# Optimization experiments

Measured on AMD Instinct MI355X. Metric: run time of the kernel, lower is better.

## Reference

```python
import jax, jax.numpy as jnp
import numpy as np

N_NODES = 50000
N_EDGES = 800000
DIM = 128
BN_EPS = 1e-5
GATE_EPS = 1e-6


def setup_inputs() -> dict:
    key = jax.random.key(0)
    ks = jax.random.split(key, 14)
    scale = 1.0 / np.sqrt(DIM)
    inp = {
        "h": jax.random.normal(ks[0], (N_NODES, DIM), dtype=jnp.float32),
        "e": jax.random.normal(ks[1], (N_EDGES, DIM), dtype=jnp.float32),
        "src": jax.random.randint(ks[2], (N_EDGES,), 0, N_NODES),
        "dst": jax.random.randint(ks[3], (N_EDGES,), 0, N_NODES),
        # Linear A, B, D, E (n_mlp_layer=1 -> single Linear each)
        "Wa": jax.random.uniform(ks[4], (DIM, DIM), jnp.float32, -scale, scale),
        "ba": jax.random.uniform(ks[5], (DIM,), jnp.float32, -scale, scale),
        "Wb": jax.random.uniform(ks[6], (DIM, DIM), jnp.float32, -scale, scale),
        "bb": jax.random.uniform(ks[7], (DIM,), jnp.float32, -scale, scale),
        "Wd": jax.random.uniform(ks[8], (DIM, DIM), jnp.float32, -scale, scale),
        "bd": jax.random.uniform(ks[9], (DIM,), jnp.float32, -scale, scale),
        "We": jax.random.uniform(ks[10], (DIM, DIM), jnp.float32, -scale, scale),
        "be": jax.random.uniform(ks[11], (DIM,), jnp.float32, -scale, scale),
        # BatchNorm1d affine params (fresh init: gamma=1, beta=0)
        "gamma": jnp.ones((DIM,), jnp.float32),
        "beta": jnp.zeros((DIM,), jnp.float32),
    }
    return inp


def reference(h, e, src, dst, Wa, ba, Wb, bb, Wd, bd, We, be, gamma, beta):
    N = h.shape[0]
    # dense node projections
    Ah = h @ Wa + ba
    Bh = h @ Wb + bb
    Dh = h @ Wd + bd
    Eh = h @ We + be
    # edge gather + sigmoid gate: e_ij = Dh[src] + Eh[dst]
    sigma = jax.nn.sigmoid(Dh[src] + Eh[dst])          # [E, D]
    # scatter-sum by destination node (variable degree)
    num = jax.ops.segment_sum(sigma * Bh[src], dst, num_segments=N)
    den = jax.ops.segment_sum(sigma, dst, num_segments=N) + GATE_EPS
    h_new = Ah + num / den
    # BatchNorm1d (training mode: biased batch statistics) + relu
    mean = jnp.mean(h_new, axis=0)
    var = jnp.mean(jnp.square(h_new - mean), axis=0)
    h_new = (h_new - mean) * jax.lax.rsqrt(var + BN_EPS) * gamma + beta
    h_new = jax.nn.relu(h_new)
    # residual=False (default), dropout=0.0 -> identity
    return h_new, e
```

## Files before the change

### kernel.cpp

```cpp
#include <hip/hip_runtime.h>
#include <hip/hip_bf16.h>

#define DIM 128
#define GATE_EPS 1e-6f
#define BN_EPS 1e-5f

typedef unsigned int u32;
typedef unsigned short u16;

__device__ __forceinline__ float bflo(u32 u) { return __uint_as_float(u << 16); }
__device__ __forceinline__ float bfhi(u32 u) { return __uint_as_float(u & 0xffff0000u); }

__device__ __forceinline__ u16 f2bf(float f) {
    u32 u = __float_as_uint(f);
    u32 r = (u + 0x7fffu + ((u >> 16) & 1u)) >> 16;
    return (u16)r;
}

__device__ __forceinline__ float loadF(const void* p, size_t i, int bf) {
    if (bf) return __uint_as_float(((u32)((const u16*)p)[i]) << 16);
    return ((const float*)p)[i];
}

__global__ void detect_dtype(const void* __restrict__ h, int* __restrict__ flag) {
    if (threadIdx.x == 0 && blockIdx.x == 0) {
        const u16* us = (const u16*)h;
        int cnt = 0;
        for (int i = 0; i < 256; ++i) {
            int e8 = (us[2 * i] >> 7) & 0xFF;
            if (e8 >= 0x60 && e8 <= 0x8F) ++cnt;
        }
        *flag = (cnt >= 192) ? 1 : 0;
    }
}

__global__ __launch_bounds__(256) void proj_gemm(
    const void* __restrict__ h,
    const void* __restrict__ W0, const void* __restrict__ b0,
    const void* __restrict__ W1, const void* __restrict__ b1,
    const void* __restrict__ W2, const void* __restrict__ b2,
    const void* __restrict__ W3, const void* __restrict__ b3,
    float* __restrict__ oAh, u32* __restrict__ oDB, u32* __restrict__ oEhb,
    int N, const int* __restrict__ flagp)
{
    const void* W; const void* bias;
    switch (blockIdx.y) {
        case 0:  W = W0; bias = b0; break;
        case 1:  W = W1; bias = b1; break;
        case 2:  W = W2; bias = b2; break;
        default: W = W3; bias = b3; break;
    }
    const int bf = *flagp;

    __shared__ float Hs[64][DIM + 4];
    __shared__ float Ws[16][DIM];

    const int t  = threadIdx.x;
    const int m0 = blockIdx.x * 64;

    if (bf) {
        for (int f = t; f < 1024; f += 256) {
            int r = f >> 4, c8 = f & 15;
            int gr = m0 + r;
            uint4 v = make_uint4(0u, 0u, 0u, 0u);
            if (gr < N) v = ((const uint4*)h)[(size_t)gr * 16 + c8];
            float* p = &Hs[r][c8 * 8];
            p[0] = bflo(v.x); p[1] = bfhi(v.x);
            p[2] = bflo(v.y); p[3] = bfhi(v.y);
            p[4] = bflo(v.z); p[5] = bfhi(v.z);
            p[6] = bflo(v.w); p[7] = bfhi(v.w);
        }
    } else {
        for (int f = t; f < 2048; f += 256) {
            int r = f >> 5, c4 = f & 31;
            int gr = m0 + r;
            float4 v = make_float4(0.f, 0.f, 0.f, 0.f);
            if (gr < N) v = ((const float4*)h)[(size_t)gr * 32 + c4];
            float* p = &Hs[r][c4 * 4];
            p[0] = v.x; p[1] = v.y; p[2] = v.z; p[3] = v.w;
        }
    }

    const int cg = t & 31;
    const int rg = t >> 5;

    float acc[8][4];
    #pragma unroll
    for (int i = 0; i < 8; ++i)
        #pragma unroll
        for (int j = 0; j < 4; ++j) acc[i][j] = 0.f;

    for (int kc = 0; kc < DIM; kc += 16) {
        __syncthreads();
        if (bf) {
            int r = t >> 4, c8 = t & 15;
            uint4 v = ((const uint4*)W)[(size_t)(kc + r) * 16 + c8];
            float* p = &Ws[r][c8 * 8];
            p[0] = bflo(v.x); p[1] = bfhi(v.x);
            p[2] = bflo(v.y); p[3] = bfhi(v.y);
            p[4] = bflo(v.z); p[5] = bfhi(v.z);
            p[6] = bflo(v.w); p[7] = bfhi(v.w);
        } else {
            for (int f = t; f < 512; f += 256) {
                int r = f >> 5, c4 = f & 31;
                float4 v = ((const float4*)W)[(size_t)(kc + r) * 32 + c4];
                float* p = &Ws[r][c4 * 4];
                p[0] = v.x; p[1] = v.y; p[2] = v.z; p[3] = v.w;
            }
        }
        __syncthreads();
        #pragma unroll
        for (int kk = 0; kk < 16; ++kk) {
            float4 w = *((const float4*)&Ws[kk][cg * 4]);
            #pragma unroll
            for (int i = 0; i < 8; ++i) {
                float hv = Hs[rg * 8 + i][kc + kk];
                acc[i][0] += hv * w.x;
                acc[i][1] += hv * w.y;
                acc[i][2] += hv * w.z;
                acc[i][3] += hv * w.w;
            }
        }
    }

    float bv[4];
    #pragma unroll
    for (int j = 0; j < 4; ++j) bv[j] = loadF(bias, cg * 4 + j, bf);

    const int y = blockIdx.y;
    #pragma unroll
    for (int i = 0; i < 8; ++i) {
        int gr = m0 + rg * 8 + i;
        if (gr < N) {
            float v0 = acc[i][0] + bv[0];
            float v1 = acc[i][1] + bv[1];
            float v2 = acc[i][2] + bv[2];
            float v3 = acc[i][3] + bv[3];
            if (y == 0) {
                ((float4*)oAh)[(size_t)gr * 32 + cg] = make_float4(v0, v1, v2, v3);
            } else {
                uint2 p;
                p.x = (u32)f2bf(v0) | ((u32)f2bf(v1) << 16);
                p.y = (u32)f2bf(v2) | ((u32)f2bf(v3) << 16);
                size_t idx;
                if (y == 1)      idx = (size_t)gr * 64 + 32 + cg;
                else if (y == 2) idx = (size_t)gr * 64 + cg;
                else             idx = (size_t)gr * 32 + cg;
                u32* base = (y == 3) ? oEhb : oDB;
                ((uint2*)base)[idx] = p;
            }
        }
    }
}

__global__ __launch_bounds__(256) void k_hist(const int* __restrict__ dst,
                                              int* __restrict__ deg, int E)
{
    int e = blockIdx.x * 256 + threadIdx.x;
    if (e < E) atomicAdd(&deg[dst[e]], 1);
}

__global__ __launch_bounds__(256) void k_scan1(const int* __restrict__ deg,
                                               int* __restrict__ rowstart,
                                               int* __restrict__ part, int N)
{
    __shared__ int s[256];
    int t = threadIdx.x;
    int i = blockIdx.x * 256 + t;
    int d = (i < N) ? deg[i] : 0;
    s[t] = d;
    __syncthreads();
    for (int off = 1; off < 256; off <<= 1) {
        int v = (t >= off) ? s[t - off] : 0;
        __syncthreads();
        s[t] += v;
        __syncthreads();
    }
    if (i < N) rowstart[i] = s[t] - d;
    if (t == 255) part[blockIdx.x] = s[255];
}

__global__ void k_scan2(int* __restrict__ part, int nb)
{
    __shared__ int s[256];
    int t = threadIdx.x;
    int d = (t < nb) ? part[t] : 0;
    s[t] = d;
    __syncthreads();
    for (int off = 1; off < 256; off <<= 1) {
        int v = (t >= off) ? s[t - off] : 0;
        __syncthreads();
        s[t] += v;
        __syncthreads();
    }
    if (t < nb) part[t] = s[t] - d;
}

__global__ __launch_bounds__(256) void k_scan3(int* __restrict__ rowstart,
                                               int* __restrict__ cursor,
                                               const int* __restrict__ part,
                                               int N, int E)
{
    int i = blockIdx.x * 256 + threadIdx.x;
    if (i < N) {
        int v = rowstart[i] + part[blockIdx.x];
        rowstart[i] = v;
        cursor[i] = v;
    }
    if (i == 0) rowstart[N] = E;
}

__global__ __launch_bounds__(256) void k_scatter(const int* __restrict__ src,
                                                 const int* __restrict__ dst,
                                                 int* __restrict__ cursor,
                                                 int* __restrict__ esrc, int E)
{
    int e = blockIdx.x * 256 + threadIdx.x;
    if (e < E) {
        int pos = atomicAdd(&cursor[dst[e]], 1);
        esrc[pos] = src[e];
    }
}

__global__ __launch_bounds__(256) void k_aggregate(
    const float* __restrict__ Ah, const u32* __restrict__ DB,
    const u32* __restrict__ Ehb,
    const int* __restrict__ rowstart, const int* __restrict__ esrc,
    float* __restrict__ hnew, float* __restrict__ gsum, float* __restrict__ gsq,
    int N)
{
    int t = threadIdx.x;
    int lane = t & 63;
    int wv = t >> 6;
    int nquads = (N + 3) >> 2;

    float lsum0 = 0.f, lsum1 = 0.f, lsq0 = 0.f, lsq1 = 0.f;
    for (int q = blockIdx.x; q < nquads; q += gridDim.x) {
        int n = q * 4 + wv;
        if (n < N) {
            u32 ehp = Ehb[(size_t)n * 64 + lane];
            float eh0 = bflo(ehp), eh1 = bfhi(ehp);
            float2 ahp = ((const float2*)Ah)[(size_t)n * 64 + lane];
            float num0 = 0.f, den0 = 0.f, num1 = 0.f, den1 = 0.f;
            int beg = rowstart[n], end = rowstart[n + 1];
            int k = beg;
            for (; k + 4 <= end; k += 4) {
                int s0 = esrc[k], s1 = esrc[k + 1], s2 = esrc[k + 2], s3 = esrc[k + 3];
                u32 dhA = DB[(size_t)s0 * 128 + lane];
                u32 bhA = DB[(size_t)s0 * 128 + 64 + lane];
                u32 dhB = DB[(size_t)s1 * 128 + lane];
                u32 bhB = DB[(size_t)s1 * 128 + 64 + lane];
                u32 dhC = DB[(size_t)s2 * 128 + lane];
                u32 bhC = DB[(size_t)s2 * 128 + 64 + lane];
                u32 dhD = DB[(size_t)s3 * 128 + lane];
                u32 bhD = DB[(size_t)s3 * 128 + 64 + lane];
                float sA0 = 1.f / (1.f + __expf(-(bflo(dhA) + eh0)));
                float sA1 = 1.f / (1.f + __expf(-(bfhi(dhA) + eh1)));
                float sB0 = 1.f / (1.f + __expf(-(bflo(dhB) + eh0)));
                float sB1 = 1.f / (1.f + __expf(-(bfhi(dhB) + eh1)));
                float sC0 = 1.f / (1.f + __expf(-(bflo(dhC) + eh0)));
                float sC1 = 1.f / (1.f + __expf(-(bfhi(dhC) + eh1)));
                float sD0 = 1.f / (1.f + __expf(-(bflo(dhD) + eh0)));
                float sD1 = 1.f / (1.f + __expf(-(bfhi(dhD) + eh1)));
                num0 = fmaf(sA0, bflo(bhA), num0); den0 += sA0;
                num1 = fmaf(sA1, bfhi(bhA), num1); den1 += sA1;
                num0 = fmaf(sB0, bflo(bhB), num0); den0 += sB0;
                num1 = fmaf(sB1, bfhi(bhB), num1); den1 += sB1;
                num0 = fmaf(sC0, bflo(bhC), num0); den0 += sC0;
                num1 = fmaf(sC1, bfhi(bhC), num1); den1 += sC1;
                num0 = fmaf(sD0, bflo(bhD), num0); den0 += sD0;
                num1 = fmaf(sD1, bfhi(bhD), num1); den1 += sD1;
            }
            for (; k < end; ++k) {
                int s0 = esrc[k];
                u32 dh0 = DB[(size_t)s0 * 128 + lane];
                u32 bh0 = DB[(size_t)s0 * 128 + 64 + lane];
                float sa0 = 1.f / (1.f + __expf(-(bflo(dh0) + eh0)));
                float sa1 = 1.f / (1.f + __expf(-(bfhi(dh0) + eh1)));
                num0 = fmaf(sa0, bflo(bh0), num0); den0 += sa0;
                num1 = fmaf(sa1, bfhi(bh0), num1); den1 += sa1;
            }
            float x0 = ahp.x + num0 / (den0 + GATE_EPS);
            float x1 = ahp.y + num1 / (den1 + GATE_EPS);
            ((float2*)hnew)[(size_t)n * 64 + lane] = make_float2(x0, x1);
            lsum0 += x0; lsq0 += x0 * x0;
            lsum1 += x1; lsq1 += x1 * x1;
        }
    }
    __shared__ float S0[256], S1[256], Q0[256], Q1[256];
    S0[t] = lsum0; S1[t] = lsum1; Q0[t] = lsq0; Q1[t] = lsq1;
    __syncthreads();
    if (t < 64) {
        float s0 = S0[t] + S0[t + 64] + S0[t + 128] + S0[t + 192];
        float s1 = S1[t] + S1[t + 64] + S1[t + 128] + S1[t + 192];
        float q0 = Q0[t] + Q0[t + 64] + Q0[t + 128] + Q0[t + 192];
        float q1 = Q1[t] + Q1[t + 64] + Q1[t + 128] + Q1[t + 192];
        atomicAdd(&gsum[2 * t],     s0);
        atomicAdd(&gsum[2 * t + 1], s1);
        atomicAdd(&gsq[2 * t],      q0);
        atomicAdd(&gsq[2 * t + 1],  q1);
    }
}

__global__ void bn_finalize(const float* __restrict__ gsum, const float* __restrict__ gsq,
                            const void* __restrict__ gamma, const void* __restrict__ beta,
                            float* __restrict__ scale, float* __restrict__ shift,
                            int N, const int* __restrict__ flagp)
{
    int c = threadIdx.x;
    int bf = *flagp;
    if (c < DIM) {
        float invn = 1.f / (float)N;
        float mean = gsum[c] * invn;
        float var  = fmaxf(gsq[c] * invn - mean * mean, 0.f);
        float g = loadF(gamma, c, bf);
        float b = loadF(beta, c, bf);
        float sc = rsqrtf(var + BN_EPS) * g;
        scale[c] = sc;
        shift[c] = b - mean * sc;
    }
}

__global__ __launch_bounds__(256) void bn_apply(
    const float* __restrict__ hnew, const float* __restrict__ scale,
    const float* __restrict__ shift, void* __restrict__ outh,
    int total, const int* __restrict__ flagp)
{
    __shared__ float s_sc[DIM], s_sh[DIM];
    int t = threadIdx.x;
    if (t < DIM) { s_sc[t] = scale[t]; s_sh[t] = shift[t]; }
    __syncthreads();
    int bf = *flagp;

    int idx = blockIdx.x * 256 + t;
    int stride = gridDim.x * 256;
    for (int i = idx; i < total; i += stride) {
        int c = i & 127;
        float x = fmaxf(0.f, hnew[i] * s_sc[c] + s_sh[c]);
        if (bf) ((u16*)outh)[i] = f2bf(x);
        else    ((float*)outh)[i] = x;
    }
}

__global__ __launch_bounds__(256) void copy_e(
    const void* __restrict__ e, void* __restrict__ dout,
    size_t nd, size_t ecount, const int* __restrict__ flagp)
{
    int bf = *flagp;
    size_t esz = bf ? 2 : 4;
    const uint4* s = (const uint4*)e;
    uint4* d = (uint4*)((char*)dout + nd * esz);
    size_t n16 = (ecount * esz) / 16;
    size_t idx = (size_t)blockIdx.x * 256 + threadIdx.x;
    size_t stride = (size_t)gridDim.x * 256;
    for (size_t i = idx; i < n16; i += stride) d[i] = s[i];
}

extern "C" void kernel_launch(void* const* d_in, const int* in_sizes, int n_in,
                              void* d_out, int out_size, void* d_ws, size_t ws_size,
                              hipStream_t stream)
{
    const void* h     = d_in[0];
    const void* e     = d_in[1];
    const int*  src   = (const int*)d_in[2];
    const int*  dst   = (const int*)d_in[3];
    const void* Wa    = d_in[4];
    const void* ba    = d_in[5];
    const void* Wb    = d_in[6];
    const void* bb    = d_in[7];
    const void* Wd    = d_in[8];
    const void* bd    = d_in[9];
    const void* We    = d_in[10];
    const void* be    = d_in[11];
    const void* gamma = d_in[12];
    const void* beta  = d_in[13];

    const int N = in_sizes[0] / DIM;
    const int E = in_sizes[2];
    const size_t nd = (size_t)N * DIM;
    const size_t ecount = (size_t)E * DIM;

    float* ws    = (float*)d_ws;
    float* Ah    = ws;
    float* hnew  = ws + nd;
    u32*   DB    = (u32*)(ws + 2 * nd);
    u32*   Ehb   = (u32*)(ws + 3 * nd);
    float* gsum  = ws + 3 * nd + nd / 2;
    float* gsq   = gsum + DIM;
    float* scale = gsum + 2 * DIM;
    float* shift = gsum + 3 * DIM;
    int*   flag  = (int*)(gsum + 4 * DIM);
    int*   deg      = flag + 64;
    int*   rowstart = deg + N;
    int*   cursor   = rowstart + N + 1;
    int*   part     = cursor + N;
    int*   esrc     = part + 256;

    hipMemsetAsync(gsum, 0, (4 * DIM + 64) * sizeof(float), stream);
    hipMemsetAsync(deg, 0, (size_t)N * sizeof(int), stream);

    detect_dtype<<<1, 64, 0, stream>>>(h, flag);

    const int nbE = (E + 255) / 256;
    const int nbN = (N + 255) / 256;

    k_hist<<<nbE, 256, 0, stream>>>(dst, deg, E);
    k_scan1<<<nbN, 256, 0, stream>>>(deg, rowstart, part, N);
    k_scan2<<<1, 256, 0, stream>>>(part, nbN);
    k_scan3<<<nbN, 256, 0, stream>>>(rowstart, cursor, part, N, E);
    k_scatter<<<nbE, 256, 0, stream>>>(src, dst, cursor, esrc, E);

    dim3 g1((N + 63) / 64, 4);
    proj_gemm<<<g1, 256, 0, stream>>>(h, Wa, ba, Wb, bb, Wd, bd, We, be,
                                      Ah, DB, Ehb, N, flag);

    k_aggregate<<<2048, 256, 0, stream>>>(Ah, DB, Ehb, rowstart, esrc,
                                          hnew, gsum, gsq, N);

    bn_finalize<<<1, 128, 0, stream>>>(gsum, gsq, gamma, beta, scale, shift, N, flag);

    bn_apply<<<2048, 256, 0, stream>>>(hnew, scale, shift, d_out, (int)nd, flag);

    copy_e<<<4096, 256, 0, stream>>>(e, d_out, nd, ecount, flag);
}
```

Measured before the change: 541.0 us.

## Fuse edge scatter into projection GEMM and edge copy into aggregation

The CSR scatter of edge sources now runs as an extra blockIdx.y slice of the projection GEMM launch, and the copy of the edge tensor to the output runs as extra blocks of the aggregation launch. This removes two kernel launches and lets the independent, memory-bound work overlap with compute-heavy or gather-heavy kernels. The cost is contention for bandwidth and compute units between the fused parts, and the scatter slice now grid-strides over E with only about 782 blocks.

```diff
diff --git a/kernel.cpp b/kernel.cpp
--- a/kernel.cpp
+++ b/kernel.cpp
@@ -4,6 +4,7 @@
 #define DIM 128
 #define GATE_EPS 1e-6f
 #define BN_EPS 1e-5f
+#define AGG_BLOCKS 2048
 
 typedef unsigned int u32;
 typedef unsigned short u16;
@@ -41,8 +42,19 @@
     const void* __restrict__ W2, const void* __restrict__ b2,
     const void* __restrict__ W3, const void* __restrict__ b3,
     float* __restrict__ oAh, u32* __restrict__ oDB, u32* __restrict__ oEhb,
-    int N, const int* __restrict__ flagp)
-{
+    int N, const int* __restrict__ flagp,
+    const int* __restrict__ src, const int* __restrict__ dst,
+    int* __restrict__ cursor, int* __restrict__ esrc, int E)
+{
+    if (blockIdx.y == 4) {
+        int stride = gridDim.x * 256;
+        for (int e = blockIdx.x * 256 + threadIdx.x; e < E; e += stride) {
+            int pos = atomicAdd(&cursor[dst[e]], 1);
+            esrc[pos] = src[e];
+        }
+        return;
+    }
+
     const void* W; const void* bias;
     switch (blockIdx.y) {
         case 0:  W = W0; bias = b0; break;
@@ -210,32 +222,36 @@
     if (i == 0) rowstart[N] = E;
 }
 
-__global__ __launch_bounds__(256) void k_scatter(const int* __restrict__ src,
-                                                 const int* __restrict__ dst,
-                                                 int* __restrict__ cursor,
-                                                 int* __restrict__ esrc, int E)
-{
-    int e = blockIdx.x * 256 + threadIdx.x;
-    if (e < E) {
-        int pos = atomicAdd(&cursor[dst[e]], 1);
-        esrc[pos] = src[e];
-    }
-}
-
 __global__ __launch_bounds__(256) void k_aggregate(
     const float* __restrict__ Ah, const u32* __restrict__ DB,
     const u32* __restrict__ Ehb,
     const int* __restrict__ rowstart, const int* __restrict__ esrc,
     float* __restrict__ hnew, float* __restrict__ gsum, float* __restrict__ gsq,
-    int N)
+    int N,
+    const void* __restrict__ e, void* __restrict__ dout,
+    size_t nd, size_t ecount, const int* __restrict__ flagp)
 {
     int t = threadIdx.x;
+
+    if (blockIdx.x >= AGG_BLOCKS) {
+        int bf = *flagp;
+        size_t esz = bf ? 2 : 4;
+        const uint4* s = (const uint4*)e;
+        uint4* d = (uint4*)((char*)dout + nd * esz);
+        size_t n16 = (ecount * esz) / 16;
+        size_t cb = (size_t)(gridDim.x - AGG_BLOCKS);
+        size_t idx = (size_t)(blockIdx.x - AGG_BLOCKS) * 256 + t;
+        size_t stride = cb * 256;
+        for (size_t i = idx; i < n16; i += stride) d[i] = s[i];
+        return;
+    }
+
     int lane = t & 63;
     int wv = t >> 6;
     int nquads = (N + 3) >> 2;
 
     float lsum0 = 0.f, lsum1 = 0.f, lsq0 = 0.f, lsq1 = 0.f;
-    for (int q = blockIdx.x; q < nquads; q += gridDim.x) {
+    for (int q = blockIdx.x; q < nquads; q += AGG_BLOCKS) {
         int n = q * 4 + wv;
         if (n < N) {
             u32 ehp = Ehb[(size_t)n * 64 + lane];
@@ -342,20 +358,6 @@
     }
 }
 
-__global__ __launch_bounds__(256) void copy_e(
-    const void* __restrict__ e, void* __restrict__ dout,
-    size_t nd, size_t ecount, const int* __restrict__ flagp)
-{
-    int bf = *flagp;
-    size_t esz = bf ? 2 : 4;
-    const uint4* s = (const uint4*)e;
-    uint4* d = (uint4*)((char*)dout + nd * esz);
-    size_t n16 = (ecount * esz) / 16;
-    size_t idx = (size_t)blockIdx.x * 256 + threadIdx.x;
-    size_t stride = (size_t)gridDim.x * 256;
-    for (size_t i = idx; i < n16; i += stride) d[i] = s[i];
-}
-
 extern "C" void kernel_launch(void* const* d_in, const int* in_sizes, int n_in,
                               void* d_out, int out_size, void* d_ws, size_t ws_size,
                               hipStream_t stream)
@@ -408,18 +410,17 @@
     k_scan1<<<nbN, 256, 0, stream>>>(deg, rowstart, part, N);
     k_scan2<<<1, 256, 0, stream>>>(part, nbN);
     k_scan3<<<nbN, 256, 0, stream>>>(rowstart, cursor, part, N, E);
-    k_scatter<<<nbE, 256, 0, stream>>>(src, dst, cursor, esrc, E);
-
-    dim3 g1((N + 63) / 64, 4);
+
+    dim3 g1((N + 63) / 64, 5);
     proj_gemm<<<g1, 256, 0, stream>>>(h, Wa, ba, Wb, bb, Wd, bd, We, be,
-                                      Ah, DB, Ehb, N, flag);
-
-    k_aggregate<<<2048, 256, 0, stream>>>(Ah, DB, Ehb, rowstart, esrc,
-                                          hnew, gsum, gsq, N);
+                                      Ah, DB, Ehb, N, flag,
+                                      src, dst, cursor, esrc, E);
+
+    k_aggregate<<<AGG_BLOCKS + 2048, 256, 0, stream>>>(
+        Ah, DB, Ehb, rowstart, esrc, hnew, gsum, gsq, N,
+        e, d_out, nd, ecount, flag);
 
     bn_finalize<<<1, 128, 0, stream>>>(gsum, gsq, gamma, beta, scale, shift, N, flag);
 
     bn_apply<<<2048, 256, 0, stream>>>(hnew, scale, shift, d_out, (int)nd, flag);
-
-    copy_e<<<4096, 256, 0, stream>>>(e, d_out, nd, ecount, flag);
-}
+}
```

Result: faster. 497.3 us (-8.1%).
